# Kernel optimization log

Measured on AMD Instinct MI355X. Metric: run time of the kernel, lower is better.

The kernel has to match this reference:

```python
import jax, jax.numpy as jnp
import numpy as np

B, T, K = 16, 512, 128  # batch, seq_len, num_state


def setup_inputs() -> dict:
    key = jax.random.key(0)
    k1, k2, k3 = jax.random.split(key, 3)
    transition = jax.random.normal(k1, (K, K), dtype=jnp.float32)
    emission = jax.random.normal(k2, (B, T, K), dtype=jnp.float32)
    seq_lens = jax.random.randint(k3, (B,), 1, T + 1)  # lengths in [1, T]
    return {"transition": transition, "emission": emission, "seq_lens": seq_lens}


def reference(transition, emission, seq_lens):
    # potential_normalization='none' -> identity normalize().
    # combine_potentials: log phi[b, t, y_{t-1}, y_t] = trans[y_{t-1}, y_t] + emis[b, t, y_t]
    log_pot = transition[None, None, :, :] + emission[:, :, None, :]  # [B,T,K,K]

    alpha0 = emission[:, 0, :]  # [B,K]

    def step(alpha_prev, pot_t):  # alpha_prev: [B,K], pot_t: [B,K,K]
        alpha_t = jax.nn.logsumexp(alpha_prev[:, :, None] + pot_t, axis=1)
        return alpha_t, alpha_t

    # scan over time steps 1..T-1 (time-major potentials)
    _, alphas_rest = jax.lax.scan(step, alpha0, jnp.swapaxes(log_pot[:, 1:], 0, 1))
    alpha = jnp.concatenate(
        [alpha0[:, None, :], jnp.swapaxes(alphas_rest, 0, 1)], axis=1
    )  # [B,T,K]

    # gather alpha at position seq_lens - 1 per batch element
    last = jnp.take_along_axis(alpha, (seq_lens - 1)[:, None, None], axis=1)[:, 0, :]
    log_Z = jax.nn.logsumexp(last, axis=-1)  # [B]
    return alpha, log_Z
```

## Files before the change

### kernel.cpp

```cpp
#include <hip/hip_runtime.h>
#include <math.h>

#define KDIM 128
#define TLEN 512
#define BATCH 16
#define CH_L 16
#define NCH 32
#define NMAT 31

typedef _Float16 half8 __attribute__((ext_vector_type(8)));
typedef _Float16 half4 __attribute__((ext_vector_type(4)));
typedef _Float16 half2t __attribute__((ext_vector_type(2)));
typedef float floatx4 __attribute__((ext_vector_type(4)));

#if defined(__has_builtin)
#if __has_builtin(__builtin_amdgcn_fdot2)
#define HAVE_FDOT2 1
#endif
#endif

static __device__ __forceinline__ float dot2f(half2t a, half2t b, float c) {
#ifdef HAVE_FDOT2
    return __builtin_amdgcn_fdot2(a, b, c, false);
#else
    return fmaf((float)a[0], (float)b[0], fmaf((float)a[1], (float)b[1], c));
#endif
}

static __device__ __forceinline__ float dot8(const half8 v, const float4 w, float acc) {
    const uint4 r = __builtin_bit_cast(uint4, v);
    acc = dot2f(__builtin_bit_cast(half2t, w.x), __builtin_bit_cast(half2t, r.x), acc);
    acc = dot2f(__builtin_bit_cast(half2t, w.y), __builtin_bit_cast(half2t, r.y), acc);
    acc = dot2f(__builtin_bit_cast(half2t, w.z), __builtin_bit_cast(half2t, r.z), acc);
    acc = dot2f(__builtin_bit_cast(half2t, w.w), __builtin_bit_cast(half2t, r.w), acc);
    return acc;
}

static __device__ __forceinline__ half8 gload16_asm(const _Float16* p) {
    half8 r;
    asm volatile("global_load_dwordx4 %0, %1, off" : "=v"(r) : "v"(p));
    return r;
}
static __device__ __forceinline__ float gload4_asm(const float* p) {
    float r;
    asm volatile("global_load_dword %0, %1, off" : "=v"(r) : "v"(p));
    return r;
}

#define WSN_PST   0
#define WSN_SVEC  16252928
#define WSN_AENT  16506880
#define WSN_NEED  16769024


__global__ __launch_bounds__(256, 2) void crf_chunkcols2(
    const float* __restrict__ trans, const float* __restrict__ em,
    _Float16* __restrict__ Pst, float* __restrict__ Svec)
{
    const int bid = blockIdx.x;
    const int r = bid & 7, j = bid >> 3;
    const int b = (j < NMAT) ? r : r + 8;
    const int c = (j < NMAT) ? j : j - NMAT;
    const int tid = threadIdx.x;
    const int w = tid >> 6, lane = tid & 63;
    const int quad = lane >> 4, lm = lane & 15;

    __shared__ __align__(16) _Float16 Flds[128 * 136];
    __shared__ __align__(16) _Float16 Wscr[4][4608];
    __shared__ __align__(16) float gAll[16 * KDIM];

    const int t0 = c * CH_L + 1;
    const float* emb = em + (size_t)b * TLEN * KDIM;

    {
        const int m = tid & 127, kh = tid >> 7;
        #pragma unroll
        for (int kk = 0; kk < 8; ++kk) {
            const int k0 = kh * 64 + kk * 8;
            half8 o;
            #pragma unroll
            for (int jj = 0; jj < 8; ++jj)
                o[jj] = (_Float16)__expf(trans[(k0 + jj) * KDIM + m]);
            *(half8*)&Flds[m * 136 + k0] = o;
        }
    }
    {
        const int i8 = tid * 8;
        const float4 e0 = *(const float4*)&emb[t0 * KDIM + i8];
        const float4 e1 = *(const float4*)&emb[t0 * KDIM + i8 + 4];
        float4 g0, g1;
        g0.x = __expf(e0.x); g0.y = __expf(e0.y); g0.z = __expf(e0.z); g0.w = __expf(e0.w);
        g1.x = __expf(e1.x); g1.y = __expf(e1.y); g1.z = __expf(e1.z); g1.w = __expf(e1.w);
        *(float4*)&gAll[i8] = g0;
        *(float4*)&gAll[i8 + 4] = g1;
    }
    __syncthreads();

    _Float16* Wb = Wscr[w];
    float sc[2];
    half8 Bf[4][2];

    #pragma unroll
    for (int nt = 0; nt < 2; ++nt) {
        float tv[4][8];
        float cm = 0.f;
        const int n = 32 * w + nt * 16 + lm;
        #pragma unroll
        for (int kt = 0; kt < 4; ++kt) {
            const int r0 = kt * 32 + quad * 8;
            const float4 ga = *(const float4*)&gAll[r0];
            const float4 gb = *(const float4*)&gAll[r0 + 4];
            const float gg[8] = {ga.x, ga.y, ga.z, ga.w, gb.x, gb.y, gb.z, gb.w};
            const float4 ta = *(const float4*)&trans[(size_t)n * KDIM + r0];
            const float4 tb = *(const float4*)&trans[(size_t)n * KDIM + r0 + 4];
            const float tt[8] = {ta.x, ta.y, ta.z, ta.w, tb.x, tb.y, tb.z, tb.w};
            #pragma unroll
            for (int jj = 0; jj < 8; ++jj) {
                const float v = __expf(tt[jj]) * gg[jj];
                tv[kt][jj] = v;
                cm = fmaxf(cm, v);
            }
        }
        cm = fmaxf(cm, __shfl_xor(cm, 16));
        cm = fmaxf(cm, __shfl_xor(cm, 32));
        const float ri = 1.0f / cm;
        sc[nt] = __logf(cm);
        #pragma unroll
        for (int kt = 0; kt < 4; ++kt)
            #pragma unroll
            for (int jj = 0; jj < 8; ++jj)
                Bf[kt][nt][jj] = (_Float16)(tv[kt][jj] * ri);
    }

    half8 Af[8][4];
    #pragma unroll
    for (int mt = 0; mt < 8; ++mt)
        #pragma unroll
        for (int kt = 0; kt < 4; ++kt)
            Af[mt][kt] = *(const half8*)&Flds[lm * 136 + quad * 8 + mt * 2176 + kt * 32];

    const floatx4 z4 = {0.f, 0.f, 0.f, 0.f};
    for (int it = 1; it < 16; ++it) {
        #pragma unroll
        for (int nt = 0; nt < 2; ++nt) {
            floatx4 acc[8];
            #pragma unroll
            for (int mt = 0; mt < 8; ++mt)
                acc[mt] = __builtin_amdgcn_mfma_f32_16x16x32_f16(Af[mt][0], Bf[0][nt], z4, 0, 0, 0);
            #pragma unroll
            for (int kt = 1; kt < 4; ++kt)
                #pragma unroll
                for (int mt = 0; mt < 8; ++mt)
                    acc[mt] = __builtin_amdgcn_mfma_f32_16x16x32_f16(Af[mt][kt], Bf[kt][nt], acc[mt], 0, 0, 0);

            const float* g = &gAll[it * KDIM];
            float cm = 0.f;
            #pragma unroll
            for (int mt = 0; mt < 8; ++mt) {
                const float4 gv = *(const float4*)&g[mt * 16 + quad * 4];
                floatx4 v = acc[mt];
                v.x *= gv.x; v.y *= gv.y; v.z *= gv.z; v.w *= gv.w;
                acc[mt] = v;
                cm = fmaxf(cm, fmaxf(fmaxf(v.x, v.y), fmaxf(v.z, v.w)));
            }
            cm = fmaxf(cm, __shfl_xor(cm, 16));
            cm = fmaxf(cm, __shfl_xor(cm, 32));
            const float ri = 1.0f / cm;
            sc[nt] += __logf(cm);

            if (it < 15) {
                #pragma unroll
                for (int mt = 0; mt < 8; ++mt) {
                    const floatx4 v = acc[mt];
                    half4 o;
                    o[0] = (_Float16)(v.x * ri);
                    o[1] = (_Float16)(v.y * ri);
                    o[2] = (_Float16)(v.z * ri);
                    o[3] = (_Float16)(v.w * ri);
                    *(half4*)&Wb[lm * 136 + quad * 4 + nt * 2176 + mt * 16] = o;
                }
            } else {
                #pragma unroll
                for (int mt = 0; mt < 8; ++mt) {
                    const floatx4 v = acc[mt];
                    const int ba = quad * 144 + lm + mt * 576 + nt * 16;
                    Wb[ba]       = (_Float16)(v.x * ri);
                    Wb[ba + 36]  = (_Float16)(v.y * ri);
                    Wb[ba + 72]  = (_Float16)(v.z * ri);
                    Wb[ba + 108] = (_Float16)(v.w * ri);
                }
            }
        }
        if (it < 15) {
            #pragma unroll
            for (int kt = 0; kt < 4; ++kt)
                #pragma unroll
                for (int nt = 0; nt < 2; ++nt)
                    Bf[kt][nt] = *(const half8*)&Wb[lm * 136 + quad * 8 + nt * 2176 + kt * 32];
        }
    }

    _Float16* Pc = Pst + ((size_t)(b * NMAT + c)) * 16384;
    #pragma unroll
    for (int Kl = 0; Kl < 4; ++Kl)
        #pragma unroll
        for (int hh = 0; hh < 2; ++hh) {
            const half4 lo = *(const half4*)&Wb[(2 * lane + hh) * 36 + Kl * 8];
            const half4 hi = *(const half4*)&Wb[(2 * lane + hh) * 36 + Kl * 8 + 4];
            half8 v;
            #pragma unroll
            for (int e = 0; e < 4; ++e) { v[e] = lo[e]; v[4 + e] = hi[e]; }
            const int u = (2 * (4 * w + Kl) + hh) * 64 + lane;
            *(half8*)&Pc[(size_t)u * 8] = v;
        }
    if (quad == 0) {
        float* sp = Svec + ((size_t)(b * NMAT + c)) * KDIM + 32 * w;
        sp[lm] = sc[0];
        sp[lm + 16] = sc[1];
    }
}

__global__ __launch_bounds__(256, 1) void crf_scanw8(
    const float* __restrict__ em, const _Float16* __restrict__ Pst,
    const float* __restrict__ Svec, float* __restrict__ aEnter)
{
    const int b = blockIdx.x;
    const int tid = threadIdx.x;
    const int w = tid >> 6, lane = tid & 63;

    __shared__ __align__(16) _Float16 pbuf[KDIM];
    __shared__ __align__(16) float part[4][KDIM];
    __shared__ float red[2];

    const _Float16* Pb = Pst + (size_t)b * NMAT * 16384;
    const float* svb = Svec + (size_t)b * NMAT * KDIM;
    float* aeb = aEnter + (size_t)b * NCH * KDIM;
    const int jsv = tid & 127;

    half8 PA[8], PB[8];
    float svA, svB;
    #pragma unroll
    for (int i = 0; i < 8; ++i)
        PA[i] = gload16_asm(&Pb[((8 * w + i) * 64 + lane) * 8]);
    svA = gload4_asm(&svb[jsv]);
    #pragma unroll
    for (int i = 0; i < 8; ++i)
        PB[i] = gload16_asm(&Pb[16384 + ((8 * w + i) * 64 + lane) * 8]);
    svB = gload4_asm(&svb[KDIM + jsv]);

    float lq = 0.f, L = 0.f;
    {
        float a0 = -INFINITY;
        if (tid < KDIM) a0 = em[(size_t)b * TLEN * KDIM + tid];
        float m = a0;
        #pragma unroll
        for (int o = 32; o; o >>= 1) m = fmaxf(m, __shfl_xor(m, o));
        if (w < 2 && lane == 0) red[w] = m;
        __syncthreads();
        const float mx = fmaxf(red[0], red[1]);
        if (tid < KDIM) {
            aeb[tid] = a0;
            lq = a0 - mx;
            L = mx;
        }
        __syncthreads();
    }

    auto STEP = [&](half8 (&P)[8], float& sv, int c) {
        if (c == NMAT - 1) {
            asm volatile("s_waitcnt vmcnt(0)" ::: "memory");
        } else {
            asm volatile("s_waitcnt vmcnt(9)" ::: "memory");
        }
        __builtin_amdgcn_sched_barrier(0);

        if (w < 2) {
            float m = lq + sv;
            #pragma unroll
            for (int o = 32; o; o >>= 1) m = fmaxf(m, __shfl_xor(m, o));
            if (lane == 0) red[w] = m;
        }
        __syncthreads();
        const float M = fmaxf(red[0], red[1]);
        if (w < 2)
            pbuf[tid] = (_Float16)__expf(lq + sv - M);
        __syncthreads();

        float q0 = 0.f, q1 = 0.f;
        #pragma unroll
        for (int kk = 0; kk < 4; ++kk) {
            const float4 wv = *(const float4*)&pbuf[(4 * w + kk) * 8];
            q0 = dot8(P[2 * kk + 0], wv, q0);
            q1 = dot8(P[2 * kk + 1], wv, q1);
        }
        float2 qq; qq.x = q0; qq.y = q1;
        *(float2*)&part[w][2 * lane] = qq;
        __syncthreads();

        if (tid < KDIM) {
            const float q = part[0][tid] + part[1][tid]
                          + part[2][tid] + part[3][tid];
            const float lg = __logf(q);
            aeb[(size_t)(c + 1) * KDIM + tid] = L + M + lg;
            lq = lg;
            L += M;
        }

        if (c + 2 < NMAT) {
            #pragma unroll
            for (int i = 0; i < 8; ++i)
                P[i] = gload16_asm(&Pb[(size_t)(c + 2) * 16384
                                       + ((8 * w + i) * 64 + lane) * 8]);
            sv = gload4_asm(&svb[(size_t)(c + 2) * KDIM + jsv]);
        }
    };

    for (int c = 0; c < NMAT; c += 2) {
        STEP(PA, svA, c);
        if (c + 1 < NMAT) STEP(PB, svB, c + 1);
    }
}

__global__ __launch_bounds__(64, 1) void crf_replayw(
    const float* __restrict__ trans, const float* __restrict__ em,
    const int* __restrict__ seq_lens, const float* __restrict__ aEnter,
    float* __restrict__ alpha, float* __restrict__ logZ)
{
    const int c = blockIdx.x, b = blockIdx.y;
    const int l = threadIdx.x;

    __shared__ __align__(16) _Float16 pbuf[KDIM];

    half2t Ea[64], Eb[64];
    #pragma unroll
    for (int t2 = 0; t2 < 64; ++t2) {
        const float* r0 = &trans[(2 * t2) * KDIM];
        const float* r1 = &trans[(2 * t2 + 1) * KDIM];
        half2t ea, eb;
        ea[0] = (_Float16)__expf(r0[l]);
        ea[1] = (_Float16)__expf(r1[l]);
        eb[0] = (_Float16)__expf(r0[l + 64]);
        eb[1] = (_Float16)__expf(r1[l + 64]);
        Ea[t2] = ea;
        Eb[t2] = eb;
    }

    const int len = seq_lens[b];
    const float* emb = em + (size_t)b * TLEN * KDIM;
    float* outb = alpha + (size_t)b * TLEN * KDIM;
    const float* ae = aEnter + ((size_t)b * NCH + c) * KDIM;

    float a0 = ae[l], a1 = ae[l + 64];
    if (c == 0) {
        a0 = emb[l];
        a1 = emb[l + 64];
    }
    float mx = fmaxf(a0, a1);
    #pragma unroll
    for (int o = 32; o; o >>= 1) mx = fmaxf(mx, __shfl_xor(mx, o));
    float L = mx;
    pbuf[l]      = (_Float16)__expf(a0 - L);
    pbuf[l + 64] = (_Float16)__expf(a1 - L);

    float la0 = 0.f, la1 = -INFINITY;
    if (c == 0) {
        outb[l] = a0;
        outb[l + 64] = a1;
        if (len == 1) { la0 = a0; la1 = a1; }
    }

    const int t_begin = c * CH_L + 1;
    const int t_end = (c == NCH - 1) ? (TLEN - 1) : (c * CH_L + CH_L);

    float e0 = emb[t_begin * KDIM + l];
    float e1 = emb[t_begin * KDIM + l + 64];

    for (int t = t_begin; t <= t_end; ++t) {
        float n0 = 0.f, n1 = 0.f;
        if (t < t_end) {
            n0 = emb[(t + 1) * KDIM + l];
            n1 = emb[(t + 1) * KDIM + l + 64];
        }

        float q0 = 0.f, q1 = 0.f;
        #pragma unroll
        for (int s = 0; s < 16; ++s) {
            const float4 w = *(const float4*)&pbuf[s * 8];
            const half2t p0 = __builtin_bit_cast(half2t, w.x);
            const half2t p1 = __builtin_bit_cast(half2t, w.y);
            const half2t p2 = __builtin_bit_cast(half2t, w.z);
            const half2t p3 = __builtin_bit_cast(half2t, w.w);
            q0 = dot2f(p0, Ea[4 * s + 0], q0);
            q0 = dot2f(p1, Ea[4 * s + 1], q0);
            q0 = dot2f(p2, Ea[4 * s + 2], q0);
            q0 = dot2f(p3, Ea[4 * s + 3], q0);
            q1 = dot2f(p0, Eb[4 * s + 0], q1);
            q1 = dot2f(p1, Eb[4 * s + 1], q1);
            q1 = dot2f(p2, Eb[4 * s + 2], q1);
            q1 = dot2f(p3, Eb[4 * s + 3], q1);
        }

        const float A0 = e0 + L + __logf(q0);
        const float A1 = e1 + L + __logf(q1);
        outb[t * KDIM + l] = A0;
        outb[t * KDIM + l + 64] = A1;
        if (t == len - 1) { la0 = A0; la1 = A1; }

        const float sigma = __shfl(q0, 0);
        const float ri = 1.0f / sigma;
        pbuf[l]      = (_Float16)(q0 * ri * __expf(e0));
        pbuf[l + 64] = (_Float16)(q1 * ri * __expf(e1));
        L += __logf(sigma);
        e0 = n0; e1 = n1;
    }

    const bool blockowns = (len == 1) ? (c == 0) : (((len - 2) >> 4) == c);
    if (blockowns) {
        float m2 = fmaxf(la0, la1);
        #pragma unroll
        for (int o = 32; o; o >>= 1) m2 = fmaxf(m2, __shfl_xor(m2, o));
        float e = __expf(la0 - m2) + __expf(la1 - m2);
        #pragma unroll
        for (int o = 32; o; o >>= 1) e += __shfl_xor(e, o);
        if (l == 0) logZ[b] = m2 + __logf(e);
    }
}

__global__ __launch_bounds__(256) void crf_forward_fallback(
    const float* __restrict__ trans, const float* __restrict__ em,
    const int* __restrict__ seq_lens, float* __restrict__ alpha_out,
    float* __restrict__ logZ_out)
{
    const int b = blockIdx.x;
    const int tid = threadIdx.x;
    const int j = tid & (KDIM - 1);
    const int h = tid >> 7;

    __shared__ __align__(16) float p_lds[KDIM];
    __shared__ float part[KDIM];
    __shared__ float red[8];

    float Ereg[64];
    #pragma unroll
    for (int k = 0; k < 64; ++k) Ereg[k] = __expf(trans[(h * 64 + k) * KDIM + j]);

    const int len = seq_lens[b];
    const float* emb = em + (size_t)b * TLEN * KDIM;
    float* outb = alpha_out + (size_t)b * TLEN * KDIM;

    float a = 0.f, last_a = 0.f;
    if (h == 0) {
        a = emb[j];
        outb[j] = a;
        if (len == 1) last_a = a;
    }
    for (int t = 1; t < TLEN; ++t) {
        {
            float v = (h == 0) ? a : -INFINITY;
            #pragma unroll
            for (int o = 32; o >= 1; o >>= 1) v = fmaxf(v, __shfl_xor(v, o));
            if ((tid & 63) == 0) red[tid >> 6] = v;
        }
        __syncthreads();
        const float m = fmaxf(red[0], red[1]);
        if (h == 0) p_lds[j] = __expf(a - m);
        __syncthreads();
        float em_t = 0.f;
        if (h == 0) em_t = emb[t * KDIM + j];
        float acc0 = 0.f, acc1 = 0.f, acc2 = 0.f, acc3 = 0.f;
        const float4* p4 = (const float4*)(p_lds + h * 64);
        #pragma unroll
        for (int k4 = 0; k4 < 16; ++k4) {
            float4 pv = p4[k4];
            acc0 = fmaf(pv.x, Ereg[4 * k4 + 0], acc0);
            acc1 = fmaf(pv.y, Ereg[4 * k4 + 1], acc1);
            acc2 = fmaf(pv.z, Ereg[4 * k4 + 2], acc2);
            acc3 = fmaf(pv.w, Ereg[4 * k4 + 3], acc3);
        }
        const float acc = (acc0 + acc1) + (acc2 + acc3);
        if (h == 1) part[j] = acc;
        __syncthreads();
        if (h == 0) {
            const float q = acc + part[j];
            a = em_t + m + __logf(q);
            outb[t * KDIM + j] = a;
            if (t == len - 1) last_a = a;
        }
    }
    {
        float v = (h == 0) ? last_a : -INFINITY;
        #pragma unroll
        for (int o = 32; o >= 1; o >>= 1) v = fmaxf(v, __shfl_xor(v, o));
        if ((tid & 63) == 0) red[tid >> 6] = v;
    }
    __syncthreads();
    const float m2 = fmaxf(red[0], red[1]);
    float e = (h == 0) ? __expf(last_a - m2) : 0.f;
    #pragma unroll
    for (int o = 32; o >= 1; o >>= 1) e += __shfl_xor(e, o);
    if ((tid & 63) == 0) red[4 + (tid >> 6)] = e;
    __syncthreads();
    if (tid == 0) logZ_out[b] = m2 + logf(red[4] + red[5]);
}

extern "C" void kernel_launch(void* const* d_in, const int* in_sizes, int n_in,
                              void* d_out, int out_size, void* d_ws, size_t ws_size,
                              hipStream_t stream) {
    const float* trans    = (const float*)d_in[0];
    const float* em       = (const float*)d_in[1];
    const int*   seq_lens = (const int*)d_in[2];

    float* alpha_out = (float*)d_out;
    float* logZ_out  = alpha_out + (size_t)BATCH * TLEN * KDIM;

    char* ws = (char*)d_ws;

    if (ws_size >= (size_t)WSN_NEED) {
        _Float16* Pst  = (_Float16*)(ws + WSN_PST);
        float*    Svec = (float*)(ws + WSN_SVEC);
        float*    aEnt = (float*)(ws + WSN_AENT);
        crf_chunkcols2<<<NMAT * BATCH, 256, 0, stream>>>(trans, em, Pst, Svec);
        crf_scanw8<<<BATCH, 256, 0, stream>>>(em, Pst, Svec, aEnt);
        crf_replayw<<<dim3(NCH, BATCH), 64, 0, stream>>>(trans, em, seq_lens, aEnt,
                                                         alpha_out, logZ_out);
    } else {
        crf_forward_fallback<<<BATCH, 256, 0, stream>>>(trans, em, seq_lens,
                                                        alpha_out, logZ_out);
    }
}
```

Measured before the change: 151.2 us.

## Rewrite replay kernel as 256-thread fp32 split-K and force LDS A-fragment loads

The per-chunk replay kernel moves from one 64-lane wave doing fp16 dot2 products over 128 states to a 256-thread block. Two halves each reduce 64 source states in fp32, with partial sums combined through shared memory and two barriers per step. The chunk-matrix kernel now loads its A fragments with explicit ds_read_b128 asm, followed by a full LDS wait and a scheduling barrier. The aim is more parallelism per step and better instruction scheduling in the replay stage, at the cost of per-step block synchronisation and higher register use from fp32 exp(transition) values.

```diff
diff --git a/kernel.cpp b/kernel.cpp
--- a/kernel.cpp
+++ b/kernel.cpp
@@ -46,6 +46,12 @@
     asm volatile("global_load_dword %0, %1, off" : "=v"(r) : "v"(p));
     return r;
 }
+static __device__ __forceinline__ half8 dsread16_asm(const _Float16* p) {
+    half8 r;
+    const unsigned a = (unsigned)(size_t)p;
+    asm volatile("ds_read_b128 %0, %1" : "=v"(r) : "v"(a));
+    return r;
+}
 
 #define WSN_PST   0
 #define WSN_SVEC  16252928
@@ -53,7 +59,7 @@
 #define WSN_NEED  16769024
 
 
-__global__ __launch_bounds__(256, 2) void crf_chunkcols2(
+__global__ __launch_bounds__(256, 2) void crf_chunkcols3(
     const float* __restrict__ trans, const float* __restrict__ em,
     _Float16* __restrict__ Pst, float* __restrict__ Svec)
 {
@@ -137,7 +143,9 @@
     for (int mt = 0; mt < 8; ++mt)
         #pragma unroll
         for (int kt = 0; kt < 4; ++kt)
-            Af[mt][kt] = *(const half8*)&Flds[lm * 136 + quad * 8 + mt * 2176 + kt * 32];
+            Af[mt][kt] = dsread16_asm(&Flds[lm * 136 + quad * 8 + mt * 2176 + kt * 32]);
+    asm volatile("s_waitcnt lgkmcnt(0)" ::: "memory");
+    __builtin_amdgcn_sched_barrier(0);
 
     const floatx4 z4 = {0.f, 0.f, 0.f, 0.f};
     for (int it = 1; it < 16; ++it) {
@@ -321,108 +329,101 @@
     }
 }
 
-__global__ __launch_bounds__(64, 1) void crf_replayw(
+__global__ __launch_bounds__(256, 2) void crf_replay3(
     const float* __restrict__ trans, const float* __restrict__ em,
     const int* __restrict__ seq_lens, const float* __restrict__ aEnter,
     float* __restrict__ alpha, float* __restrict__ logZ)
 {
     const int c = blockIdx.x, b = blockIdx.y;
-    const int l = threadIdx.x;
-
-    __shared__ __align__(16) _Float16 pbuf[KDIM];
-
-    half2t Ea[64], Eb[64];
-    #pragma unroll
-    for (int t2 = 0; t2 < 64; ++t2) {
-        const float* r0 = &trans[(2 * t2) * KDIM];
-        const float* r1 = &trans[(2 * t2 + 1) * KDIM];
-        half2t ea, eb;
-        ea[0] = (_Float16)__expf(r0[l]);
-        ea[1] = (_Float16)__expf(r1[l]);
-        eb[0] = (_Float16)__expf(r0[l + 64]);
-        eb[1] = (_Float16)__expf(r1[l + 64]);
-        Ea[t2] = ea;
-        Eb[t2] = eb;
-    }
+    const int tid = threadIdx.x;
+    const int j = tid & 127, h = tid >> 7;
+    const int lane = tid & 63;
+
+    __shared__ __align__(16) float p_lds[KDIM];
+    __shared__ float part[2][KDIM];
+    __shared__ float red[8];
+
+    float Ereg[64];
+    #pragma unroll
+    for (int k = 0; k < 64; ++k)
+        Ereg[k] = __expf(trans[(h * 64 + k) * KDIM + j]);
 
     const int len = seq_lens[b];
     const float* emb = em + (size_t)b * TLEN * KDIM;
     float* outb = alpha + (size_t)b * TLEN * KDIM;
-    const float* ae = aEnter + ((size_t)b * NCH + c) * KDIM;
-
-    float a0 = ae[l], a1 = ae[l + 64];
-    if (c == 0) {
-        a0 = emb[l];
-        a1 = emb[l + 64];
-    }
-    float mx = fmaxf(a0, a1);
-    #pragma unroll
-    for (int o = 32; o; o >>= 1) mx = fmaxf(mx, __shfl_xor(mx, o));
-    float L = mx;
-    pbuf[l]      = (_Float16)__expf(a0 - L);
-    pbuf[l + 64] = (_Float16)__expf(a1 - L);
-
-    float la0 = 0.f, la1 = -INFINITY;
-    if (c == 0) {
-        outb[l] = a0;
-        outb[l + 64] = a1;
-        if (len == 1) { la0 = a0; la1 = a1; }
+
+    float a0;
+    if (c == 0) a0 = emb[j];
+    else        a0 = aEnter[((size_t)b * NCH + c) * KDIM + j];
+
+    {
+        float v = a0;
+        #pragma unroll
+        for (int o = 32; o; o >>= 1) v = fmaxf(v, __shfl_xor(v, o));
+        if (lane == 0) red[tid >> 6] = v;
+    }
+    __syncthreads();
+    float L = fmaxf(red[0], red[1]);
+
+    if (h == 0) p_lds[j] = __expf(a0 - L);
+    float la = -INFINITY;
+    if (c == 0 && h == 0) {
+        outb[j] = a0;
+        if (len == 1) la = a0;
     }
 
     const int t_begin = c * CH_L + 1;
     const int t_end = (c == NCH - 1) ? (TLEN - 1) : (c * CH_L + CH_L);
 
-    float e0 = emb[t_begin * KDIM + l];
-    float e1 = emb[t_begin * KDIM + l + 64];
+    float ecur = 0.f;
+    if (h == 0) ecur = emb[t_begin * KDIM + j];
+    __syncthreads();
 
     for (int t = t_begin; t <= t_end; ++t) {
-        float n0 = 0.f, n1 = 0.f;
-        if (t < t_end) {
-            n0 = emb[(t + 1) * KDIM + l];
-            n1 = emb[(t + 1) * KDIM + l + 64];
-        }
-
-        float q0 = 0.f, q1 = 0.f;
-        #pragma unroll
-        for (int s = 0; s < 16; ++s) {
-            const float4 w = *(const float4*)&pbuf[s * 8];
-            const half2t p0 = __builtin_bit_cast(half2t, w.x);
-            const half2t p1 = __builtin_bit_cast(half2t, w.y);
-            const half2t p2 = __builtin_bit_cast(half2t, w.z);
-            const half2t p3 = __builtin_bit_cast(half2t, w.w);
-            q0 = dot2f(p0, Ea[4 * s + 0], q0);
-            q0 = dot2f(p1, Ea[4 * s + 1], q0);
-            q0 = dot2f(p2, Ea[4 * s + 2], q0);
-            q0 = dot2f(p3, Ea[4 * s + 3], q0);
-            q1 = dot2f(p0, Eb[4 * s + 0], q1);
-            q1 = dot2f(p1, Eb[4 * s + 1], q1);
-            q1 = dot2f(p2, Eb[4 * s + 2], q1);
-            q1 = dot2f(p3, Eb[4 * s + 3], q1);
-        }
-
-        const float A0 = e0 + L + __logf(q0);
-        const float A1 = e1 + L + __logf(q1);
-        outb[t * KDIM + l] = A0;
-        outb[t * KDIM + l + 64] = A1;
-        if (t == len - 1) { la0 = A0; la1 = A1; }
-
-        const float sigma = __shfl(q0, 0);
-        const float ri = 1.0f / sigma;
-        pbuf[l]      = (_Float16)(q0 * ri * __expf(e0));
-        pbuf[l + 64] = (_Float16)(q1 * ri * __expf(e1));
-        L += __logf(sigma);
-        e0 = n0; e1 = n1;
-    }
-
-    const bool blockowns = (len == 1) ? (c == 0) : (((len - 2) >> 4) == c);
-    if (blockowns) {
-        float m2 = fmaxf(la0, la1);
+        float enxt = 0.f;
+        if (h == 0 && t < t_end) enxt = emb[(t + 1) * KDIM + j];
+
+        float acc0 = 0.f, acc1 = 0.f, acc2 = 0.f, acc3 = 0.f;
+        const float4* p4 = (const float4*)(p_lds + h * 64);
+        #pragma unroll
+        for (int k4 = 0; k4 < 16; ++k4) {
+            const float4 pv = p4[k4];
+            acc0 = fmaf(pv.x, Ereg[4 * k4 + 0], acc0);
+            acc1 = fmaf(pv.y, Ereg[4 * k4 + 1], acc1);
+            acc2 = fmaf(pv.z, Ereg[4 * k4 + 2], acc2);
+            acc3 = fmaf(pv.w, Ereg[4 * k4 + 3], acc3);
+        }
+        part[h][j] = (acc0 + acc1) + (acc2 + acc3);
+        __syncthreads();
+
+        if (h == 0) {
+            const float q = part[0][j] + part[1][j];
+            const float sig = part[0][0] + part[1][0];
+            const float A = ecur + L + __logf(q);
+            outb[t * KDIM + j] = A;
+            if (t == len - 1) la = A;
+            p_lds[j] = q * (1.0f / sig) * __expf(ecur);
+            L += __logf(sig);
+        }
+        ecur = enxt;
+        __syncthreads();
+    }
+
+    const int xown = (len == 1) ? 0 : ((len - 2) >> 4);
+    if (c == xown) {
+        float m2 = la;
         #pragma unroll
         for (int o = 32; o; o >>= 1) m2 = fmaxf(m2, __shfl_xor(m2, o));
-        float e = __expf(la0 - m2) + __expf(la1 - m2);
+        if (lane == 0) red[tid >> 6] = m2;
+        __syncthreads();
+        m2 = fmaxf(fmaxf(red[0], red[1]), fmaxf(red[2], red[3]));
+        float e = (la == -INFINITY) ? 0.f : __expf(la - m2);
         #pragma unroll
         for (int o = 32; o; o >>= 1) e += __shfl_xor(e, o);
-        if (l == 0) logZ[b] = m2 + __logf(e);
+        if (lane == 0) red[4 + (tid >> 6)] = e;
+        __syncthreads();
+        if (tid == 0)
+            logZ[b] = m2 + __logf(red[4] + red[5] + red[6] + red[7]);
     }
 }
 
@@ -519,10 +520,10 @@
         _Float16* Pst  = (_Float16*)(ws + WSN_PST);
         float*    Svec = (float*)(ws + WSN_SVEC);
         float*    aEnt = (float*)(ws + WSN_AENT);
-        crf_chunkcols2<<<NMAT * BATCH, 256, 0, stream>>>(trans, em, Pst, Svec);
+        crf_chunkcols3<<<NMAT * BATCH, 256, 0, stream>>>(trans, em, Pst, Svec);
         crf_scanw8<<<BATCH, 256, 0, stream>>>(em, Pst, Svec, aEnt);
-        crf_replayw<<<dim3(NCH, BATCH), 64, 0, stream>>>(trans, em, seq_lens, aEnt,
-                                                         alpha_out, logZ_out);
+        crf_replay3<<<dim3(NCH, BATCH), 256, 0, stream>>>(trans, em, seq_lens, aEnt,
+                                                          alpha_out, logZ_out);
     } else {
         crf_forward_fallback<<<BATCH, 256, 0, stream>>>(trans, em, seq_lens,
                                                         alpha_out, logZ_out);
```

After: 153.5 us. About the same (+1.5%).
